# Kernel tuning notes

Measured on AMD Instinct MI355X. Metric: run time of the kernel, lower is better.

The kernel has to match this reference:

```python
import jax, jax.numpy as jnp
import numpy as np

# dims: B batch, T timesteps, S sensors, O obs_dim, E obs_embed_dim, P pe_emb_dim, A inter-sensor attn dim
B, T, S, O, E, P, A, OUT = 64, 128, 64, 4, 64, 16, 10, 128


def positional_encoding(times, pe_dim):
    # standard sinusoidal PE over continuous times -> (B, T, pe_dim)
    # (sin block then cos block; mathematically same frequencies as interleaved torch version)
    freq = jnp.exp(jnp.arange(0, pe_dim, 2, dtype=jnp.float32) * (-jnp.log(10000.0) / pe_dim))
    ang = times[..., None] * freq  # (B, T, pe_dim//2)
    return jnp.concatenate([jnp.sin(ang), jnp.cos(ang)], axis=-1)


def setup_inputs() -> dict:
    key = jax.random.key(0)
    ks = jax.random.split(key, 16)
    x = jax.random.normal(ks[0], (B, T, S, O), dtype=jnp.float32)
    times = jnp.sort(jax.random.uniform(ks[1], (B, T), dtype=jnp.float32) * 100.0, axis=1)
    mask = (jax.random.uniform(ks[2], (B, T, S), dtype=jnp.float32) < 0.8).astype(jnp.float32)
    s = 0.1  # param scale (module inits near zero; use small random for a meaningful baseline)
    params = dict(
        obs_emb_weights=jax.random.normal(ks[3], (S, O, E), dtype=jnp.float32) * s,
        inter_sensor_attn_weights=jax.random.normal(ks[4], (S, A), dtype=jnp.float32) * s,
        W_recv=jax.random.normal(ks[5], (E, A + P), dtype=jnp.float32) * s,
        b_recv=jax.random.normal(ks[6], (A + P,), dtype=jnp.float32) * s,
        bidir_weights=jax.random.normal(ks[7], (S, E), dtype=jnp.float32) * s,
        W_q=jax.random.normal(ks[8], (E + P, A), dtype=jnp.float32) * s,
        b_q=jax.random.normal(ks[9], (A,), dtype=jnp.float32) * s,
        W_k=jax.random.normal(ks[10], (E + P, A), dtype=jnp.float32) * s,
        b_k=jax.random.normal(ks[11], (A,), dtype=jnp.float32) * s,
        W_s=jax.random.normal(ks[12], (T, 1), dtype=jnp.float32) * s,
        b_s=jax.random.normal(ks[13], (1,), dtype=jnp.float32) * s,
        W_emb=jax.random.normal(ks[14], (E + P, OUT), dtype=jnp.float32) * s,
        b_emb=jax.random.normal(ks[15], (OUT,), dtype=jnp.float32) * s,
    )
    return dict(x=x, times=times, mask=mask, **params)


def reference(x, times, mask, obs_emb_weights, inter_sensor_attn_weights,
              W_recv, b_recv, bidir_weights, W_q, b_q, W_k, b_k,
              W_s, b_s, W_emb, b_emb):
    b, t, s, _ = x.shape
    e = obs_emb_weights.shape[-1]
    pe_dim = W_recv.shape[1] - inter_sensor_attn_weights.shape[1]

    # per-sensor observation embedding, masked
    h = jax.nn.relu(jnp.einsum('btso,soe->btse', x, obs_emb_weights))
    h = h * mask[..., None]

    pe = positional_encoding(times, pe_dim)                      # (B,T,P)
    pe_rep = jnp.broadcast_to(pe[:, :, None, :], (b, t, s, pe_dim))

    # inter-sensor attention alpha: (B,T,S_recv,S_send)
    attn_cat = jnp.concatenate(
        [jnp.broadcast_to(inter_sensor_attn_weights[None, None], (b, t, s, inter_sensor_attn_weights.shape[1])),
         pe_rep], axis=-1)                                        # (B,T,S,A+P)
    h_map = h @ W_recv + b_recv                                   # (B,T,S,A+P)
    alpha = jax.nn.relu(jnp.einsum('btid,btjd->btij', h_map, attn_cat))

    bidir = bidir_weights @ bidir_weights.T                       # (S,S)

    def propagate(h_in, adj):
        # fused form of: (h.unsqueeze(2) * (bidir*alpha*adj)[...,None]).sum(3)
        w = bidir[None, None] * alpha * adj[:, None]              # (B,T,S,S)
        return jax.nn.relu(jnp.einsum('btij,btje->btie', w, h_in))

    adj1 = jnp.ones((b, s, s), dtype=x.dtype)
    h = propagate(h, adj1)
    adj2 = adj1 * (alpha.sum(axis=1) / mask.sum(axis=1)[..., None])  # (B,S,S)
    h = propagate(h, adj2)

    H = jnp.concatenate([h, pe_rep], axis=-1).transpose(0, 2, 1, 3)  # (B,S,T,E+P)

    # temporal self-attention
    Q = H @ W_q + b_q                                             # (B,S,T,A)
    K = H @ W_k + b_k
    scale = 1.0 / jnp.sqrt(jnp.float32(e + pe_dim))
    beta = jnp.einsum('bsta,bsua->bstu', Q, K) * scale            # (B,S,T,T)
    beta = (beta @ W_s)[..., 0] + b_s[0]                          # (B,S,T)
    beta = jax.nn.softmax(beta, axis=-1)

    out = jnp.einsum('bst,bstd->bsd', beta, H) @ W_emb + b_emb    # (B,S,OUT)
    return out
```

## Files before the change

### kernel.cpp

```cpp
#include <hip/hip_runtime.h>
#include <hip/hip_bf16.h>


typedef unsigned short u16;
typedef unsigned int u32;
typedef __attribute__((ext_vector_type(8))) short short8;
typedef __attribute__((ext_vector_type(4))) float f32x4;

#define OFF_BIDIR 131072
#define OFF_MS    135168
#define OFF_ADJ   139264
#define OFF_BRP   401408
#define OFF_ST    401424
#define BOFF_WRT  1638464u
#define BOFF_CATX 1642560u
#define BOFF_PEH  1644608u
#define BOFF_ADJS 1906752u
#define BOFF_V    2431040u
#define BOFF_W1   3479616u
#define BOFF_HT   70588480u
#define BOFF_HH   137697344u

__device__ __forceinline__ u16 f2bf(float f){
  __hip_bfloat16 h = __float2bfloat16(f);
  union { __hip_bfloat16 h; u16 u; } v; v.h = h; return v.u;
}
__device__ __forceinline__ u32 pk2bf(float lo, float hi){
  __hip_bfloat162 h = __float22bfloat162_rn(float2{lo, hi});
  union { __hip_bfloat162 h; u32 u; } v; v.h = h; return v.u;
}
__device__ __forceinline__ float bf2f(u16 h){
  union { u32 u; float f; } v; v.u = ((u32)h) << 16; return v.f;
}

__global__ void k_pre(const float* __restrict__ times, const float* __restrict__ mask,
                      const float* __restrict__ Wb, const float* __restrict__ Wrecv,
                      const float* __restrict__ brecv, const float* __restrict__ battn,
                      float* __restrict__ ws_f, char* __restrict__ ws_b) {
  __shared__ float peL[32][17];
  __shared__ float wpe[64][17];
  __shared__ float pm[4][64];
  const int blk = blockIdx.x, tid = threadIdx.x;
  u16* wrt  = (u16*)(ws_b + BOFF_WRT);
  u16* catx = (u16*)(ws_b + BOFF_CATX);
  u16* peh  = (u16*)(ws_b + BOFF_PEH);
  u16* vv   = (u16*)(ws_b + BOFF_V);
  float* ST = ws_f + OFF_ST;
  if (blk < 256) {
    #pragma unroll
    for (int r = 0; r < 2; ++r) {
      int id = blk * 512 + r * 256 + tid;
      int bt = id >> 4, k = id & 15;
      float tv = times[bt];
      int kk = k & 7;
      float fr = expf(-(float)kk * 1.1512925465f);
      float ang = tv * fr;
      float v = (k < 8) ? sinf(ang) : cosf(ang);
      peh[id] = f2bf(v);
      peL[r*16 + (tid >> 4)][k] = v;
    }
    #pragma unroll
    for (int q = 0; q < 4; ++q) {
      int idx = q * 256 + tid;
      wpe[idx >> 4][idx & 15] = Wrecv[(idx >> 4)*26 + 10 + (idx & 15)];
    }
    __syncthreads();
    {
      int btl = tid >> 3, e0 = (tid & 7) * 8;
      float acc[8];
      #pragma unroll
      for (int i = 0; i < 8; ++i) acc[i] = 0.f;
      #pragma unroll
      for (int k = 0; k < 16; ++k) {
        float p = peL[btl][k];
        #pragma unroll
        for (int i = 0; i < 8; ++i) acc[i] += wpe[e0 + i][k] * p;
      }
      u32* dst = (u32*)&vv[(blk*32 + btl)*64 + e0];
      #pragma unroll
      for (int p = 0; p < 4; ++p) dst[p] = pk2bf(acc[2*p], acc[2*p+1]);
      if (tid < 32) {
        float s = 0.f;
        #pragma unroll
        for (int k = 0; k < 16; ++k) s += brecv[10 + k] * peL[tid][k];
        ST[blk*32 + tid] = s;
      }
    }
  } else if (blk < 260) {
    float* bidir = ws_f + OFF_BIDIR;
    int q = blk - 256;
    for (int rr = 0; rr < 4; ++rr) {
      int idx = (q*4 + rr) * 256 + tid;
      int i = idx >> 6, j = idx & 63;
      float acc = 0.f;
      for (int e = 0; e < 64; ++e) acc += Wb[i*64+e] * Wb[j*64+e];
      bidir[idx] = acc;
    }
  } else if (blk == 260) {
    for (int r = 0; r < 8; ++r) {
      int idx = r * 256 + tid;
      int d = idx >> 6, e = idx & 63;
      wrt[idx] = (d < 26) ? f2bf(Wrecv[e*26 + d]) : (u16)0;
    }
    if (tid < 16) ws_f[OFF_BRP + tid] = (tid < 10) ? brecv[tid] : 0.f;
    #pragma unroll
    for (int i = 0; i < 4; ++i) {
      int idx = i * 256 + tid;
      int j = idx >> 4, d = idx & 15;
      catx[idx] = (d < 10) ? f2bf(battn[j*10 + d]) : ((d == 10) ? f2bf(1.f) : (u16)0);
    }
  } else if (blk < 325) {
    int b = blk - 261;
    int i = tid & 63, q = tid >> 6;
    float s = 0.f;
    for (int t = q*32; t < q*32 + 32; ++t) s += mask[(b*128 + t)*64 + i];
    pm[q][i] = s;
    __syncthreads();
    if (tid < 64)
      (ws_f + OFF_MS)[b*64 + tid] =
          1.0f / (pm[0][tid] + pm[1][tid] + pm[2][tid] + pm[3][tid]);
  } else {
    int zb = blk - 325;
    float4 z4 = {0.f, 0.f, 0.f, 0.f};
    float4* dst = (float4*)(ws_f + OFF_ADJ);
    #pragma unroll
    for (int r = 0; r < 16; ++r) dst[zb*4096 + r*256 + tid] = z4;
  }
}

__global__ __launch_bounds__(256)
void k_adj(const float* __restrict__ x, const float* __restrict__ mask,
           const float* __restrict__ Wobs, float* __restrict__ ws_f,
           char* __restrict__ ws_b) {
  __shared__ __align__(16) u16 hA[64][72];
  __shared__ __align__(16) u16 hmA[64][24];

  const int tid = threadIdx.x;
  const int b = blockIdx.y, tc = blockIdx.x;
  const int w = tid >> 6, l = tid & 63, lr = l & 15, lq = l >> 4, kb = lq * 8;
  const int i0 = 16*w + lq*4;
  const u16* wrt  = (const u16*)(ws_b + BOFF_WRT);
  const u16* catx = (const u16*)(ws_b + BOFF_CATX);
  const u16* vv   = (const u16*)(ws_b + BOFF_V);
  const float* brp = ws_f + OFF_BRP;
  const float* ST = ws_f + OFF_ST;
  const float* bidirG = ws_f + OFF_BIDIR;
  float* adj = ws_f + OFF_ADJ;

  const short8 z8 = (short8){0,0,0,0,0,0,0,0};
  const bool lowk = (lq < 2);
  short8 w0 = z8, w1 = z8;
  if (lr < 10) {
    const u16* wr = wrt + lr * 64;
    w0 = *(const short8*)&wr[kb];
    w1 = *(const short8*)&wr[32 + kb];
  }
  short8 bc[4];
  #pragma unroll
  for (int n = 0; n < 4; ++n)
    bc[n] = lowk ? *(const short8*)&catx[(16*n + lr)*16 + lq*8] : z8;
  float4 bv = *(const float4*)&brp[lq*4];
  float bidirR[4][4];
  #pragma unroll
  for (int n = 0; n < 4; ++n)
    #pragma unroll
    for (int reg = 0; reg < 4; ++reg)
      bidirR[n][reg] = bidirG[((i0+reg) << 6) + 16*n + lr];

  f32x4 asum[4];
  #pragma unroll
  for (int n = 0; n < 4; ++n) asum[n] = (f32x4){0.f,0.f,0.f,0.f};

  const int e4 = tid & 15, sg = tid >> 4;

  for (int tt = 0; tt < 8; ++tt) {
    int t = tc * 8 + tt;
    int base = b * 128 + t;
    short8 av0 = z8, av1 = z8;
    if (lr == 10) {
      av0 = *(const short8*)&vv[base*64 + kb];
      av1 = *(const short8*)&vv[base*64 + 32 + kb];
    }
    float st = ST[base];
    {
      float4 mk4 = *(const float4*)&mask[base*64 + sg*4];
      float mks[4] = {mk4.x, mk4.y, mk4.z, mk4.w};
      u16 hv[4][4];
      #pragma unroll
      for (int si = 0; si < 4; ++si) {
        int s = sg*4 + si;
        float4 xv = *(const float4*)&x[base*256 + s*4];
        float xo[4] = {xv.x, xv.y, xv.z, xv.w};
        float ax = 0.f, ay = 0.f, az = 0.f, aw = 0.f;
        #pragma unroll
        for (int o = 0; o < 4; ++o) {
          float4 wv = *(const float4*)&Wobs[(s*4+o)*64 + e4*4];
          ax += xo[o]*wv.x; ay += xo[o]*wv.y; az += xo[o]*wv.z; aw += xo[o]*wv.w;
        }
        float mk = mks[si];
        uint2 p;
        p.x = pk2bf(fmaxf(ax,0.f)*mk, fmaxf(ay,0.f)*mk);
        p.y = pk2bf(fmaxf(az,0.f)*mk, fmaxf(aw,0.f)*mk);
        *(uint2*)&hA[s][e4*4] = p;
        hv[si][0] = (u16)p.x; hv[si][1] = (u16)(p.x >> 16);
        hv[si][2] = (u16)p.y; hv[si][3] = (u16)(p.y >> 16);
      }
      u16* hTg = (u16*)(ws_b + BOFF_HT) + (size_t)base * 4096;
      #pragma unroll
      for (int k = 0; k < 4; ++k) {
        uint2 q;
        q.x = (u32)hv[0][k] | ((u32)hv[1][k] << 16);
        q.y = (u32)hv[2][k] | ((u32)hv[3][k] << 16);
        *(uint2*)&hTg[(e4*4 + k)*64 + sg*4] = q;
      }
    }
    __syncthreads();
    {
      short8 a0 = (lr < 10) ? w0 : av0;
      short8 a1 = (lr < 10) ? w1 : av1;
      f32x4 acc = (f32x4){0.f,0.f,0.f,0.f};
      short8 b0 = *(const short8*)&hA[16*w + lr][kb];
      short8 b1 = *(const short8*)&hA[16*w + lr][32 + kb];
      acc = __builtin_amdgcn_mfma_f32_16x16x32_bf16(a0, b0, acc, 0, 0, 0);
      acc = __builtin_amdgcn_mfma_f32_16x16x32_bf16(a1, b1, acc, 0, 0, 0);
      uint2 qq;
      qq.x = pk2bf(acc[0]+bv.x, acc[1]+bv.y);
      qq.y = pk2bf(acc[2]+bv.z, acc[3]+bv.w);
      *(uint2*)&hmA[16*w + lr][lq*4] = qq;
    }
    __syncthreads();
    {
      short8 am = lowk ? *(const short8*)&hmA[16*w + lr][lq*8] : z8;
      u32 w1u[8];
      #pragma unroll
      for (int n = 0; n < 4; ++n) {
        f32x4 z = (f32x4){st, st, st, st};
        z = __builtin_amdgcn_mfma_f32_16x16x32_bf16(am, bc[n], z, 0, 0, 0);
        float w1v[4];
        #pragma unroll
        for (int reg = 0; reg < 4; ++reg) {
          float al = fmaxf(z[reg], 0.f);
          asum[n][reg] += al;
          w1v[reg] = al * bidirR[n][reg];
        }
        w1u[2*n]   = pk2bf(w1v[0], w1v[1]);
        w1u[2*n+1] = pk2bf(w1v[2], w1v[3]);
      }
      u16* w1g = (u16*)(ws_b + BOFF_W1) + (size_t)base * 4096 + tid * 16;
      uint4 A, B;
      A.x = w1u[0]; A.y = w1u[1]; A.z = w1u[2]; A.w = w1u[3];
      B.x = w1u[4]; B.y = w1u[5]; B.z = w1u[6]; B.w = w1u[7];
      *(uint4*)&w1g[0] = A;
      *(uint4*)&w1g[8] = B;
    }
    __syncthreads();
  }
  #pragma unroll
  for (int n = 0; n < 4; ++n) {
    #pragma unroll
    for (int reg = 0; reg < 4; ++reg) {
      int i = i0 + reg, j = 16*n + lr;
      atomicAdd(&adj[((size_t)b << 12) + (i << 6) + j], asum[n][reg]);
    }
  }
}

__global__ __launch_bounds__(256)
void k_scale(const float* __restrict__ ws_f, char* __restrict__ ws_b) {
  const int b = blockIdx.x, tid = threadIdx.x;
  const float* adj = ws_f + OFF_ADJ + (size_t)b * 4096;
  const float* msI = ws_f + OFF_MS + b * 64;
  u16* as_ = (u16*)(ws_b + BOFF_ADJS) + (size_t)b * 4096;
  #pragma unroll
  for (int k = 0; k < 16; ++k) {
    int idx = k * 256 + tid;
    int i = idx >> 6;
    as_[idx] = f2bf(adj[idx] * msI[i]);
  }
}

__global__ __launch_bounds__(256, 4)
void k_main(const float* __restrict__ ws_f, const char* __restrict__ ws_b,
            u16* __restrict__ Hh) {
  __shared__ __align__(16) char smem[36864];
  u16 (*h1L)[72] = (u16 (*)[72])(smem);
  u16 (*hT)[72]  = (u16 (*)[72])(smem + 9216);
  u16 (*wA)[72]  = (u16 (*)[72])(smem + 18432);
  u16 (*adjS)[72]= (u16 (*)[72])(smem + 27648);

  const int tid = threadIdx.x;
  const int t = blockIdx.x, b = blockIdx.y;
  const int w = tid >> 6, l = tid & 63, lr = l & 15, lq = l >> 4, kb = lq * 8;
  const int base = b * 128 + t;
  const int i0 = 16*w + lq*4;

  const uint4* ag = (const uint4*)(ws_b + BOFF_ADJS + (size_t)b * 8192);
  uint4 g0 = ag[2*tid], g1 = ag[2*tid + 1];
  const uint4* hp = (const uint4*)((const u16*)(ws_b + BOFF_HT) + (size_t)base * 4096);
  uint4 hv0 = hp[2*tid], hv1 = hp[2*tid + 1];
  const uint4* wp = (const uint4*)((const u16*)(ws_b + BOFF_W1) + (size_t)base * 4096);
  uint4 wp0 = wp[2*tid], wp1 = wp[2*tid + 1];

  {
    int r = tid >> 2, c = (tid & 3) * 16;
    *(uint4*)&hT[r][c]     = hv0;
    *(uint4*)&hT[r][c + 8] = hv1;
    u32 q[8] = {wp0.x, wp0.y, wp0.z, wp0.w, wp1.x, wp1.y, wp1.z, wp1.w};
    #pragma unroll
    for (int n = 0; n < 4; ++n) {
      int j = 16*n + lr;
      u32 lo = q[2*n], hi = q[2*n+1];
      wA[i0+0][j] = (u16)lo; wA[i0+1][j] = (u16)(lo >> 16);
      wA[i0+2][j] = (u16)hi; wA[i0+3][j] = (u16)(hi >> 16);
    }
    int idx0 = 2*tid, idx1 = 2*tid + 1;
    *(uint4*)&adjS[idx0 >> 3][(idx0 & 7) * 8] = g0;
    *(uint4*)&adjS[idx1 >> 3][(idx1 & 7) * 8] = g1;
  }
  __syncthreads();

  {
    short8 aw0 = *(const short8*)&wA[16*w + lr][kb];
    short8 aw1 = *(const short8*)&wA[16*w + lr][32 + kb];
    #pragma unroll
    for (int n = 0; n < 4; ++n) {
      f32x4 acc = (f32x4){0.f,0.f,0.f,0.f};
      short8 b0 = *(const short8*)&hT[16*n + lr][kb];
      short8 b1 = *(const short8*)&hT[16*n + lr][32 + kb];
      acc = __builtin_amdgcn_mfma_f32_16x16x32_bf16(aw0, b0, acc, 0, 0, 0);
      acc = __builtin_amdgcn_mfma_f32_16x16x32_bf16(aw1, b1, acc, 0, 0, 0);
      int e = 16*n + lr;
      uint2 pp;
      pp.x = pk2bf(fmaxf(acc[0],0.f), fmaxf(acc[1],0.f));
      pp.y = pk2bf(fmaxf(acc[2],0.f), fmaxf(acc[3],0.f));
      *(uint2*)&h1L[e][i0] = pp;
    }
  }
  __syncthreads();

  {
    int row = 16*w + lr;
    union { short8 v; u16 h[8]; u32 u[4]; } uw0, uw1, ud0, ud1, oa, ob;
    uw0.v = *(const short8*)&wA[row][kb];
    uw1.v = *(const short8*)&wA[row][32 + kb];
    ud0.v = *(const short8*)&adjS[row][kb];
    ud1.v = *(const short8*)&adjS[row][32 + kb];
    #pragma unroll
    for (int k = 0; k < 4; ++k) {
      oa.u[k] = pk2bf(bf2f(uw0.h[2*k])*bf2f(ud0.h[2*k]),
                      bf2f(uw0.h[2*k+1])*bf2f(ud0.h[2*k+1]));
      ob.u[k] = pk2bf(bf2f(uw1.h[2*k])*bf2f(ud1.h[2*k]),
                      bf2f(uw1.h[2*k+1])*bf2f(ud1.h[2*k+1]));
    }
    short8 a20 = oa.v, a21 = ob.v;
    size_t obase = ((size_t)b * 64) * 8192 + (size_t)t * 64;
    #pragma unroll
    for (int n = 0; n < 4; ++n) {
      f32x4 acc = (f32x4){0.f,0.f,0.f,0.f};
      short8 b0 = *(const short8*)&h1L[16*n + lr][kb];
      short8 b1 = *(const short8*)&h1L[16*n + lr][32 + kb];
      acc = __builtin_amdgcn_mfma_f32_16x16x32_bf16(a20, b0, acc, 0, 0, 0);
      acc = __builtin_amdgcn_mfma_f32_16x16x32_bf16(a21, b1, acc, 0, 0, 0);
      int e = 16*n + lr;
      u32 p0 = pk2bf(fmaxf(acc[0],0.f), fmaxf(acc[1],0.f));
      u32 p1 = pk2bf(fmaxf(acc[2],0.f), fmaxf(acc[3],0.f));
      Hh[obase + (size_t)(i0+0) * 8192 + e] = (u16)p0;
      Hh[obase + (size_t)(i0+1) * 8192 + e] = (u16)(p0 >> 16);
      Hh[obase + (size_t)(i0+2) * 8192 + e] = (u16)p1;
      Hh[obase + (size_t)(i0+3) * 8192 + e] = (u16)(p1 >> 16);
    }
  }
}

#define HTP 82

__global__ __launch_bounds__(512)
void k_attn(const char* __restrict__ ws_b, const u16* __restrict__ Hh,
            const float* __restrict__ Wq, const float* __restrict__ bq,
            const float* __restrict__ Wk, const float* __restrict__ bk,
            const float* __restrict__ Ws, const float* __restrict__ bs,
            const float* __restrict__ Wemb, const float* __restrict__ bemb,
            float* __restrict__ out) {
  __shared__ u16 Ht[128][HTP];
  __shared__ u16 peB[128][18];
  __shared__ float wsL[128];
  __shared__ float pA[6][80];
  __shared__ float pK[8][10];
  __shared__ float qvL[80];
  __shared__ float pC[4][128];
  __shared__ float bb[128];
  __shared__ float red[4];
  __shared__ float cstL, sWL;

  const int tid = threadIdx.x;
  const int s = blockIdx.x, b = blockIdx.y;
  const float scale = 0.111803398875f;
  const u16* peh = (const u16*)(ws_b + BOFF_PEH);

  const u16* src = Hh + ((size_t)b * 64 + s) * 8192;
  #pragma unroll
  for (int r = 0; r < 2; ++r) {
    int id = r * 512 + tid;
    int tt = id >> 3, c = (id & 7) * 8;
    uint4 q = *(const uint4*)&src[tt * 64 + c];
    u32* dst = (u32*)&Ht[tt][c];
    dst[0] = q.x; dst[1] = q.y; dst[2] = q.z; dst[3] = q.w;
  }
  #pragma unroll
  for (int r = 0; r < 2; ++r) {
    int id = r * 512 + tid;
    u32 pv = ((const u32*)(peh + (size_t)b * 2048))[id];
    *(u32*)&peB[id >> 3][(id & 7) * 2] = pv;
  }
  if (tid < 128) wsL[tid] = Ws[tid];
  __syncthreads();

  if (tid < 480) {
    int d = tid % 80, c = tid / 80;
    int t0 = c * 22, t1 = (t0 + 22 > 128) ? 128 : t0 + 22;
    float a0 = 0.f, a1 = 0.f, a2 = 0.f, a3 = 0.f;
    int t = t0;
    if (d < 64) {
      for (; t + 4 <= t1; t += 4) {
        a0 += wsL[t]   * bf2f(Ht[t][d]);
        a1 += wsL[t+1] * bf2f(Ht[t+1][d]);
        a2 += wsL[t+2] * bf2f(Ht[t+2][d]);
        a3 += wsL[t+3] * bf2f(Ht[t+3][d]);
      }
      for (; t < t1; ++t) a0 += wsL[t] * bf2f(Ht[t][d]);
    } else {
      int k = d - 64;
      for (; t + 4 <= t1; t += 4) {
        a0 += wsL[t]   * bf2f(peB[t][k]);
        a1 += wsL[t+1] * bf2f(peB[t+1][k]);
        a2 += wsL[t+2] * bf2f(peB[t+2][k]);
        a3 += wsL[t+3] * bf2f(peB[t+3][k]);
      }
      for (; t < t1; ++t) a0 += wsL[t] * bf2f(peB[t][k]);
    }
    pA[c][d] = (a0 + a1) + (a2 + a3);
  } else if (tid == 480) {
    float a0 = 0.f, a1 = 0.f, a2 = 0.f, a3 = 0.f;
    for (int t = 0; t < 128; t += 4) {
      a0 += wsL[t]; a1 += wsL[t+1]; a2 += wsL[t+2]; a3 += wsL[t+3];
    }
    sWL = (a0 + a1) + (a2 + a3);
  }
  __syncthreads();

  if (tid < 80) {
    int a = tid % 10, c = tid / 10;
    float a0 = 0.f, a1 = 0.f;
    #pragma unroll
    for (int i = 0; i < 10; i += 2) {
      int d = c * 10 + i;
      float h0 = pA[0][d] + pA[1][d] + pA[2][d] + pA[3][d] + pA[4][d] + pA[5][d];
      float h1 = pA[0][d+1] + pA[1][d+1] + pA[2][d+1] + pA[3][d+1] + pA[4][d+1] + pA[5][d+1];
      a0 += h0 * Wk[d * 10 + a];
      a1 += h1 * Wk[(d+1) * 10 + a];
    }
    pK[c][a] = a0 + a1;
  }
  __syncthreads();

  if (tid <= 80) {
    float kt[10];
    #pragma unroll
    for (int a = 0; a < 10; ++a) {
      float acc = sWL * bk[a];
      #pragma unroll
      for (int c = 0; c < 8; ++c) acc += pK[c][a];
      kt[a] = acc;
    }
    if (tid < 80) {
      float a0 = 0.f, a1 = 0.f;
      #pragma unroll
      for (int a = 0; a < 10; a += 2) {
        a0 += Wq[tid * 10 + a] * kt[a];
        a1 += Wq[tid * 10 + a + 1] * kt[a + 1];
      }
      qvL[tid] = a0 + a1;
    } else {
      float cq = 0.f;
      #pragma unroll
      for (int a = 0; a < 10; ++a) cq += bq[a] * kt[a];
      cstL = scale * cq + bs[0];
    }
  }
  __syncthreads();

  {
    int t = tid & 127, q = tid >> 7;
    float a0 = 0.f, a1 = 0.f, a2 = 0.f, a3 = 0.f;
    const u32* row = (const u32*)&Ht[t][0];
    if (q == 0) {
      #pragma unroll
      for (int i = 0; i < 10; i += 2) {
        u32 p0 = row[i], p1 = row[i+1];
        a0 += bf2f((u16)p0) * qvL[2*i]   + bf2f((u16)(p0 >> 16)) * qvL[2*i+1];
        a1 += bf2f((u16)p1) * qvL[2*i+2] + bf2f((u16)(p1 >> 16)) * qvL[2*i+3];
      }
    } else if (q == 1) {
      #pragma unroll
      for (int i = 10; i < 20; i += 2) {
        u32 p0 = row[i], p1 = row[i+1];
        a0 += bf2f((u16)p0) * qvL[2*i]   + bf2f((u16)(p0 >> 16)) * qvL[2*i+1];
        a1 += bf2f((u16)p1) * qvL[2*i+2] + bf2f((u16)(p1 >> 16)) * qvL[2*i+3];
      }
    } else if (q == 2) {
      #pragma unroll
      for (int i = 20; i < 32; i += 4) {
        u32 p0 = row[i], p1 = row[i+1], p2 = row[i+2], p3 = row[i+3];
        a0 += bf2f((u16)p0) * qvL[2*i]   + bf2f((u16)(p0 >> 16)) * qvL[2*i+1];
        a1 += bf2f((u16)p1) * qvL[2*i+2] + bf2f((u16)(p1 >> 16)) * qvL[2*i+3];
        a2 += bf2f((u16)p2) * qvL[2*i+4] + bf2f((u16)(p2 >> 16)) * qvL[2*i+5];
        a3 += bf2f((u16)p3) * qvL[2*i+6] + bf2f((u16)(p3 >> 16)) * qvL[2*i+7];
      }
    } else {
      #pragma unroll
      for (int k = 0; k < 16; k += 4) {
        a0 += bf2f(peB[t][k])   * qvL[64 + k];
        a1 += bf2f(peB[t][k+1]) * qvL[65 + k];
        a2 += bf2f(peB[t][k+2]) * qvL[66 + k];
        a3 += bf2f(peB[t][k+3]) * qvL[67 + k];
      }
    }
    pC[q][t] = (a0 + a1) + (a2 + a3);
  }
  __syncthreads();

  if (tid < 128) {
    float v = scale * (pC[0][tid] + pC[1][tid] + pC[2][tid] + pC[3][tid]) + cstL;
    bb[tid] = v;
    float mm = v;
    #pragma unroll
    for (int off = 32; off; off >>= 1) mm = fmaxf(mm, __shfl_xor(mm, off));
    if ((tid & 63) == 0) red[tid >> 6] = mm;
  }
  __syncthreads();
  float mx = fmaxf(red[0], red[1]);
  if (tid < 128) {
    float ev = expf(bb[tid] - mx);
    bb[tid] = ev;
    float ss = ev;
    #pragma unroll
    for (int off = 32; off; off >>= 1) ss += __shfl_xor(ss, off);
    if ((tid & 63) == 0) red[2 + (tid >> 6)] = ss;
  }
  __syncthreads();

  if (tid < 480) {
    int d = tid % 80, c = tid / 80;
    int t0 = c * 22, t1 = (t0 + 22 > 128) ? 128 : t0 + 22;
    float a0 = 0.f, a1 = 0.f, a2 = 0.f, a3 = 0.f;
    int t = t0;
    if (d < 64) {
      for (; t + 4 <= t1; t += 4) {
        a0 += bb[t]   * bf2f(Ht[t][d]);
        a1 += bb[t+1] * bf2f(Ht[t+1][d]);
        a2 += bb[t+2] * bf2f(Ht[t+2][d]);
        a3 += bb[t+3] * bf2f(Ht[t+3][d]);
      }
      for (; t < t1; ++t) a0 += bb[t] * bf2f(Ht[t][d]);
    } else {
      int k = d - 64;
      for (; t + 4 <= t1; t += 4) {
        a0 += bb[t]   * bf2f(peB[t][k]);
        a1 += bb[t+1] * bf2f(peB[t+1][k]);
        a2 += bb[t+2] * bf2f(peB[t+2][k]);
        a3 += bb[t+3] * bf2f(peB[t+3][k]);
      }
      for (; t < t1; ++t) a0 += bb[t] * bf2f(peB[t][k]);
    }
    pA[c][d] = (a0 + a1) + (a2 + a3);
  }
  __syncthreads();

  {
    int o = tid & 127, q = tid >> 7;
    int d0 = q * 20;
    float a0 = 0.f, a1 = 0.f, a2 = 0.f, a3 = 0.f;
    #pragma unroll
    for (int i = 0; i < 20; i += 4) {
      int d = d0 + i;
      float h0 = pA[0][d]   + pA[1][d]   + pA[2][d]   + pA[3][d]   + pA[4][d]   + pA[5][d];
      float h1 = pA[0][d+1] + pA[1][d+1] + pA[2][d+1] + pA[3][d+1] + pA[4][d+1] + pA[5][d+1];
      float h2 = pA[0][d+2] + pA[1][d+2] + pA[2][d+2] + pA[3][d+2] + pA[4][d+2] + pA[5][d+2];
      float h3 = pA[0][d+3] + pA[1][d+3] + pA[2][d+3] + pA[3][d+3] + pA[4][d+3] + pA[5][d+3];
      a0 += h0 * Wemb[d * 128 + o];
      a1 += h1 * Wemb[(d+1) * 128 + o];
      a2 += h2 * Wemb[(d+2) * 128 + o];
      a3 += h3 * Wemb[(d+3) * 128 + o];
    }
    pC[q][o] = (a0 + a1) + (a2 + a3);
  }
  __syncthreads();
  if (tid < 128) {
    float rdenom = 1.0f / (red[2] + red[3]);
    out[(((size_t)b * 64 + s) << 7) + tid] =
        bemb[tid] + (pC[0][tid] + pC[1][tid] + pC[2][tid] + pC[3][tid]) * rdenom;
  }
}

extern "C" void kernel_launch(void* const* d_in, const int* in_sizes, int n_in,
                              void* d_out, int out_size, void* d_ws, size_t ws_size,
                              hipStream_t stream) {
  (void)in_sizes; (void)n_in; (void)out_size; (void)ws_size;
  const float* x     = (const float*)d_in[0];
  const float* times = (const float*)d_in[1];
  const float* mask  = (const float*)d_in[2];
  const float* Wobs  = (const float*)d_in[3];
  const float* Wattn = (const float*)d_in[4];
  const float* Wrecv = (const float*)d_in[5];
  const float* brecv = (const float*)d_in[6];
  const float* Wb    = (const float*)d_in[7];
  const float* Wq    = (const float*)d_in[8];
  const float* bq    = (const float*)d_in[9];
  const float* Wk    = (const float*)d_in[10];
  const float* bk    = (const float*)d_in[11];
  const float* Ws    = (const float*)d_in[12];
  const float* bs    = (const float*)d_in[13];
  const float* Wemb  = (const float*)d_in[14];
  const float* bemb  = (const float*)d_in[15];
  float* out = (float*)d_out;
  float* ws_f = (float*)d_ws;
  char* ws_b = (char*)d_ws;
  u16* Hh = (u16*)(ws_b + BOFF_HH);

  k_pre<<<341, 256, 0, stream>>>(times, mask, Wb, Wrecv, brecv, Wattn, ws_f, ws_b);
  k_adj<<<dim3(16, 64), 256, 0, stream>>>(x, mask, Wobs, ws_f, ws_b);
  k_scale<<<64, 256, 0, stream>>>(ws_f, ws_b);
  k_main<<<dim3(128, 64), 256, 0, stream>>>(ws_f, ws_b, Hh);
  k_attn<<<dim3(64, 64), 512, 0, stream>>>(ws_b, Hh, Wq, bq, Wk, bk, Ws, bs, Wemb, bemb, out);
}
```

Baseline: 137.0 us.

## Coalesce hT workspace stores and double k_adj grid for more parallelism

k_adj now writes each thread's 4x4 bf16 transposed tile of h as two contiguous 16-byte stores in a thread-major layout, replacing four strided 8-byte scatter stores. k_main is changed to match, doing the transpose when it places the data in LDS. Separately, k_adj handles 4 timesteps per block instead of 8 and its grid doubles to 32x64, which adds blocks and occupancy. The cost is more uncoalesced-style 8-byte LDS writes in k_main and some extra per-block setup work in k_adj.

```diff
diff --git a/kernel.cpp b/kernel.cpp
--- a/kernel.cpp
+++ b/kernel.cpp
@@ -173,8 +173,8 @@
 
   const int e4 = tid & 15, sg = tid >> 4;
 
-  for (int tt = 0; tt < 8; ++tt) {
-    int t = tc * 8 + tt;
+  for (int tt = 0; tt < 4; ++tt) {
+    int t = tc * 4 + tt;
     int base = b * 128 + t;
     short8 av0 = z8, av1 = z8;
     if (lr == 10) {
@@ -205,14 +205,16 @@
         hv[si][0] = (u16)p.x; hv[si][1] = (u16)(p.x >> 16);
         hv[si][2] = (u16)p.y; hv[si][3] = (u16)(p.y >> 16);
       }
-      u16* hTg = (u16*)(ws_b + BOFF_HT) + (size_t)base * 4096;
-      #pragma unroll
-      for (int k = 0; k < 4; ++k) {
-        uint2 q;
-        q.x = (u32)hv[0][k] | ((u32)hv[1][k] << 16);
-        q.y = (u32)hv[2][k] | ((u32)hv[3][k] << 16);
-        *(uint2*)&hTg[(e4*4 + k)*64 + sg*4] = q;
-      }
+      u16* hTg = (u16*)(ws_b + BOFF_HT) + (size_t)base * 4096 + tid * 16;
+      u32 lo0 = (u32)hv[0][0] | ((u32)hv[1][0] << 16), hi0 = (u32)hv[2][0] | ((u32)hv[3][0] << 16);
+      u32 lo1 = (u32)hv[0][1] | ((u32)hv[1][1] << 16), hi1 = (u32)hv[2][1] | ((u32)hv[3][1] << 16);
+      u32 lo2 = (u32)hv[0][2] | ((u32)hv[1][2] << 16), hi2 = (u32)hv[2][2] | ((u32)hv[3][2] << 16);
+      u32 lo3 = (u32)hv[0][3] | ((u32)hv[1][3] << 16), hi3 = (u32)hv[2][3] | ((u32)hv[3][3] << 16);
+      uint4 A, B;
+      A.x = lo0; A.y = hi0; A.z = lo1; A.w = hi1;
+      B.x = lo2; B.y = hi2; B.z = lo3; B.w = hi3;
+      *(uint4*)&hTg[0] = A;
+      *(uint4*)&hTg[8] = B;
     }
     __syncthreads();
     {
@@ -302,9 +304,15 @@
   uint4 wp0 = wp[2*tid], wp1 = wp[2*tid + 1];
 
   {
-    int r = tid >> 2, c = (tid & 3) * 16;
-    *(uint4*)&hT[r][c]     = hv0;
-    *(uint4*)&hT[r][c + 8] = hv1;
+    const int e4 = tid & 15, sg = tid >> 4;
+    uint2 p0; p0.x = hv0.x; p0.y = hv0.y;
+    uint2 p1; p1.x = hv0.z; p1.y = hv0.w;
+    uint2 p2; p2.x = hv1.x; p2.y = hv1.y;
+    uint2 p3; p3.x = hv1.z; p3.y = hv1.w;
+    *(uint2*)&hT[e4*4 + 0][sg*4] = p0;
+    *(uint2*)&hT[e4*4 + 1][sg*4] = p1;
+    *(uint2*)&hT[e4*4 + 2][sg*4] = p2;
+    *(uint2*)&hT[e4*4 + 3][sg*4] = p3;
     u32 q[8] = {wp0.x, wp0.y, wp0.z, wp0.w, wp1.x, wp1.y, wp1.z, wp1.w};
     #pragma unroll
     for (int n = 0; n < 4; ++n) {
@@ -628,7 +636,7 @@
   u16* Hh = (u16*)(ws_b + BOFF_HH);
 
   k_pre<<<341, 256, 0, stream>>>(times, mask, Wb, Wrecv, brecv, Wattn, ws_f, ws_b);
-  k_adj<<<dim3(16, 64), 256, 0, stream>>>(x, mask, Wobs, ws_f, ws_b);
+  k_adj<<<dim3(32, 64), 256, 0, stream>>>(x, mask, Wobs, ws_f, ws_b);
   k_scale<<<64, 256, 0, stream>>>(ws_f, ws_b);
   k_main<<<dim3(128, 64), 256, 0, stream>>>(ws_f, ws_b, Hh);
   k_attn<<<dim3(64, 64), 512, 0, stream>>>(ws_b, Hh, Wq, bq, Wk, bk, Ws, bs, Wemb, bemb, out);
```

New measurement: 149.1 us. 8.9% more time.

## Recompute transposed obs embedding in k_main and replace adj atomics with partials

Applied to the files above, without the earlier changes.

Stops k_adj from writing the transposed per-timestep embedding (about 64 MB of bf16) to global memory. k_main now recomputes it from x, mask and Wobs straight into shared memory. The atomicAdd accumulation of the adjacency sums is replaced by per-time-chunk partial buffers that k_scale reduces, so k_pre no longer needs its zeroing blocks. This trades a large global round-trip for a small recompute in k_main, and atomic contention for a 16-way reduction read.

```diff
diff --git a/kernel.cpp b/kernel.cpp
--- a/kernel.cpp
+++ b/kernel.cpp
@@ -9,7 +9,6 @@
 
 #define OFF_BIDIR 131072
 #define OFF_MS    135168
-#define OFF_ADJ   139264
 #define OFF_BRP   401408
 #define OFF_ST    401424
 #define BOFF_WRT  1638464u
@@ -18,7 +17,7 @@
 #define BOFF_ADJS 1906752u
 #define BOFF_V    2431040u
 #define BOFF_W1   3479616u
-#define BOFF_HT   70588480u
+#define BOFF_ADJP 70588480u
 #define BOFF_HH   137697344u
 
 __device__ __forceinline__ u16 f2bf(float f){
@@ -109,7 +108,7 @@
       int j = idx >> 4, d = idx & 15;
       catx[idx] = (d < 10) ? f2bf(battn[j*10 + d]) : ((d == 10) ? f2bf(1.f) : (u16)0);
     }
-  } else if (blk < 325) {
+  } else {
     int b = blk - 261;
     int i = tid & 63, q = tid >> 6;
     float s = 0.f;
@@ -119,12 +118,6 @@
     if (tid < 64)
       (ws_f + OFF_MS)[b*64 + tid] =
           1.0f / (pm[0][tid] + pm[1][tid] + pm[2][tid] + pm[3][tid]);
-  } else {
-    int zb = blk - 325;
-    float4 z4 = {0.f, 0.f, 0.f, 0.f};
-    float4* dst = (float4*)(ws_f + OFF_ADJ);
-    #pragma unroll
-    for (int r = 0; r < 16; ++r) dst[zb*4096 + r*256 + tid] = z4;
   }
 }
 
@@ -145,7 +138,6 @@
   const float* brp = ws_f + OFF_BRP;
   const float* ST = ws_f + OFF_ST;
   const float* bidirG = ws_f + OFF_BIDIR;
-  float* adj = ws_f + OFF_ADJ;
 
   const short8 z8 = (short8){0,0,0,0,0,0,0,0};
   const bool lowk = (lq < 2);
@@ -185,7 +177,6 @@
     {
       float4 mk4 = *(const float4*)&mask[base*64 + sg*4];
       float mks[4] = {mk4.x, mk4.y, mk4.z, mk4.w};
-      u16 hv[4][4];
       #pragma unroll
       for (int si = 0; si < 4; ++si) {
         int s = sg*4 + si;
@@ -202,16 +193,6 @@
         p.x = pk2bf(fmaxf(ax,0.f)*mk, fmaxf(ay,0.f)*mk);
         p.y = pk2bf(fmaxf(az,0.f)*mk, fmaxf(aw,0.f)*mk);
         *(uint2*)&hA[s][e4*4] = p;
-        hv[si][0] = (u16)p.x; hv[si][1] = (u16)(p.x >> 16);
-        hv[si][2] = (u16)p.y; hv[si][3] = (u16)(p.y >> 16);
-      }
-      u16* hTg = (u16*)(ws_b + BOFF_HT) + (size_t)base * 4096;
-      #pragma unroll
-      for (int k = 0; k < 4; ++k) {
-        uint2 q;
-        q.x = (u32)hv[0][k] | ((u32)hv[1][k] << 16);
-        q.y = (u32)hv[2][k] | ((u32)hv[3][k] << 16);
-        *(uint2*)&hTg[(e4*4 + k)*64 + sg*4] = q;
       }
     }
     __syncthreads();
@@ -255,12 +236,13 @@
     }
     __syncthreads();
   }
-  #pragma unroll
-  for (int n = 0; n < 4; ++n) {
-    #pragma unroll
-    for (int reg = 0; reg < 4; ++reg) {
-      int i = i0 + reg, j = 16*n + lr;
-      atomicAdd(&adj[((size_t)b << 12) + (i << 6) + j], asum[n][reg]);
+  {
+    float* adjP = (float*)(ws_b + BOFF_ADJP) + (((size_t)tc * 64 + b) << 12) + tid * 16;
+    #pragma unroll
+    for (int n = 0; n < 4; ++n) {
+      float4 A;
+      A.x = asum[n][0]; A.y = asum[n][1]; A.z = asum[n][2]; A.w = asum[n][3];
+      *(float4*)&adjP[n * 4] = A;
     }
   }
 }
@@ -268,20 +250,37 @@
 __global__ __launch_bounds__(256)
 void k_scale(const float* __restrict__ ws_f, char* __restrict__ ws_b) {
   const int b = blockIdx.x, tid = threadIdx.x;
-  const float* adj = ws_f + OFF_ADJ + (size_t)b * 4096;
+  const int w = tid >> 6, l = tid & 63, lr = l & 15, lq = l >> 4;
+  const int i0 = 16*w + lq*4;
   const float* msI = ws_f + OFF_MS + b * 64;
   u16* as_ = (u16*)(ws_b + BOFF_ADJS) + (size_t)b * 4096;
-  #pragma unroll
-  for (int k = 0; k < 16; ++k) {
-    int idx = k * 256 + tid;
-    int i = idx >> 6;
-    as_[idx] = f2bf(adj[idx] * msI[i]);
-  }
+
+  float S[16];
+  #pragma unroll
+  for (int k = 0; k < 16; ++k) S[k] = 0.f;
+  for (int tc = 0; tc < 16; ++tc) {
+    const float4* src = (const float4*)
+        ((const float*)(ws_b + BOFF_ADJP) + (((size_t)tc * 64 + b) << 12) + tid * 16);
+    #pragma unroll
+    for (int n = 0; n < 4; ++n) {
+      float4 v = src[n];
+      S[n*4+0] += v.x; S[n*4+1] += v.y; S[n*4+2] += v.z; S[n*4+3] += v.w;
+    }
+  }
+  float msr[4];
+  #pragma unroll
+  for (int reg = 0; reg < 4; ++reg) msr[reg] = msI[i0 + reg];
+  #pragma unroll
+  for (int n = 0; n < 4; ++n)
+    #pragma unroll
+    for (int reg = 0; reg < 4; ++reg)
+      as_[(i0 + reg) * 64 + 16*n + lr] = f2bf(S[n*4 + reg] * msr[reg]);
 }
 
 __global__ __launch_bounds__(256, 4)
-void k_main(const float* __restrict__ ws_f, const char* __restrict__ ws_b,
-            u16* __restrict__ Hh) {
+void k_main(const float* __restrict__ x, const float* __restrict__ mask,
+            const float* __restrict__ Wobs, const float* __restrict__ ws_f,
+            const char* __restrict__ ws_b, u16* __restrict__ Hh) {
   __shared__ __align__(16) char smem[36864];
   u16 (*h1L)[72] = (u16 (*)[72])(smem);
   u16 (*hT)[72]  = (u16 (*)[72])(smem + 9216);
@@ -296,15 +295,38 @@
 
   const uint4* ag = (const uint4*)(ws_b + BOFF_ADJS + (size_t)b * 8192);
   uint4 g0 = ag[2*tid], g1 = ag[2*tid + 1];
-  const uint4* hp = (const uint4*)((const u16*)(ws_b + BOFF_HT) + (size_t)base * 4096);
-  uint4 hv0 = hp[2*tid], hv1 = hp[2*tid + 1];
   const uint4* wp = (const uint4*)((const u16*)(ws_b + BOFF_W1) + (size_t)base * 4096);
   uint4 wp0 = wp[2*tid], wp1 = wp[2*tid + 1];
 
   {
-    int r = tid >> 2, c = (tid & 3) * 16;
-    *(uint4*)&hT[r][c]     = hv0;
-    *(uint4*)&hT[r][c + 8] = hv1;
+    const int e4 = tid & 15, sg = tid >> 4;
+    float4 mk4 = *(const float4*)&mask[base*64 + sg*4];
+    float mks[4] = {mk4.x, mk4.y, mk4.z, mk4.w};
+    u16 hv[4][4];
+    #pragma unroll
+    for (int si = 0; si < 4; ++si) {
+      int s = sg*4 + si;
+      float4 xv = *(const float4*)&x[base*256 + s*4];
+      float xo[4] = {xv.x, xv.y, xv.z, xv.w};
+      float ax = 0.f, ay = 0.f, az = 0.f, aw = 0.f;
+      #pragma unroll
+      for (int o = 0; o < 4; ++o) {
+        float4 wv = *(const float4*)&Wobs[(s*4+o)*64 + e4*4];
+        ax += xo[o]*wv.x; ay += xo[o]*wv.y; az += xo[o]*wv.z; aw += xo[o]*wv.w;
+      }
+      float mk = mks[si];
+      u32 plo = pk2bf(fmaxf(ax,0.f)*mk, fmaxf(ay,0.f)*mk);
+      u32 phi = pk2bf(fmaxf(az,0.f)*mk, fmaxf(aw,0.f)*mk);
+      hv[si][0] = (u16)plo; hv[si][1] = (u16)(plo >> 16);
+      hv[si][2] = (u16)phi; hv[si][3] = (u16)(phi >> 16);
+    }
+    #pragma unroll
+    for (int k = 0; k < 4; ++k) {
+      uint2 q;
+      q.x = (u32)hv[0][k] | ((u32)hv[1][k] << 16);
+      q.y = (u32)hv[2][k] | ((u32)hv[3][k] << 16);
+      *(uint2*)&hT[e4*4 + k][sg*4] = q;
+    }
     u32 q[8] = {wp0.x, wp0.y, wp0.z, wp0.w, wp1.x, wp1.y, wp1.z, wp1.w};
     #pragma unroll
     for (int n = 0; n < 4; ++n) {
@@ -627,9 +649,9 @@
   char* ws_b = (char*)d_ws;
   u16* Hh = (u16*)(ws_b + BOFF_HH);
 
-  k_pre<<<341, 256, 0, stream>>>(times, mask, Wb, Wrecv, brecv, Wattn, ws_f, ws_b);
+  k_pre<<<325, 256, 0, stream>>>(times, mask, Wb, Wrecv, brecv, Wattn, ws_f, ws_b);
   k_adj<<<dim3(16, 64), 256, 0, stream>>>(x, mask, Wobs, ws_f, ws_b);
   k_scale<<<64, 256, 0, stream>>>(ws_f, ws_b);
-  k_main<<<dim3(128, 64), 256, 0, stream>>>(ws_f, ws_b, Hh);
+  k_main<<<dim3(128, 64), 256, 0, stream>>>(x, mask, Wobs, ws_f, ws_b, Hh);
   k_attn<<<dim3(64, 64), 512, 0, stream>>>(ws_b, Hh, Wq, bq, Wk, bk, Ws, bs, Wemb, bemb, out);
 }
```

New measurement: 144.3 us. 5.3% more time.
